# Kernel tuning notes

Hardware: AMD Instinct MI355X
Metric: run time of the kernel (lower is better)

Reference implementation:

```python
import jax, jax.numpy as jnp
import numpy as np

ALPHA = 0.2  # LeakyReLU negative slope


def _head(x, W, b, a, eye):
    # x: [B,N,F], W: [F,D], a: [2D,1], eye: [N,N] identity
    h = x @ W + b                                   # [B,N,D]
    D = W.shape[1]
    # additive attention: score[i,j] = leakyrelu(a_l . h_i + a_r . h_j)
    s = jax.nn.leaky_relu(h @ a[:D] + jnp.swapaxes(h @ a[D:], 1, 2), ALPHA)  # [B,N,N]
    s = jnp.where(eye > 0, -jnp.inf, s)             # mask diagonal (adj_identity)
    p = jax.nn.softmax(s, axis=-1) + eye            # softmax then add identity
    return jax.nn.elu(p @ h)                        # [B,N,D]


def setup_inputs() -> dict:
    key = jax.random.key(0)
    ks = jax.random.split(key, 16)
    B, N, F_IN, HID, HEADS = 8, 2048, 256, 256, 2
    D = HID // HEADS
    inp = {
        "x": jax.random.normal(ks[0], (B, N, F_IN), dtype=jnp.float32),
        "edges": jax.random.randint(ks[1], (B, N), 0, N, dtype=jnp.int64),
    }
    i = 2
    for layer in range(2):
        fin = F_IN if layer == 0 else HID
        for head in range(HEADS):
            inp[f"W_{layer}_{head}"] = jax.random.normal(ks[i], (fin, D), dtype=jnp.float32) * (1.0 / np.sqrt(fin)); i += 1
            inp[f"b_{layer}_{head}"] = jnp.zeros((D,), dtype=jnp.float32)
            inp[f"a_{layer}_{head}"] = jax.random.normal(ks[i], (2 * D, 1), dtype=jnp.float32) * 0.1; i += 1
    return inp


def reference(x, edges, W_0_0, b_0_0, a_0_0, W_0_1, b_0_1, a_0_1,
              W_1_0, b_1_0, a_1_0, W_1_1, b_1_1, a_1_1):
    N = x.shape[1]
    eye = jnp.eye(N, dtype=x.dtype)
    layers = [
        [(W_0_0, b_0_0, a_0_0), (W_0_1, b_0_1, a_0_1)],
        [(W_1_0, b_1_0, a_1_0), (W_1_1, b_1_1, a_1_1)],
    ]
    for heads in layers:
        x = jnp.concatenate([_head(x, W, b, a, eye) for (W, b, a) in heads], axis=-1)
    return x
```

## Files before the change

kernel.cpp:

```cpp
#include <hip/hip_runtime.h>
#include <math.h>

#define ALPHA_SLOPE 0.2f

typedef _Float16 f16;
typedef f16 f16x4 __attribute__((ext_vector_type(4)));
typedef f16 f16x8 __attribute__((ext_vector_type(8)));
typedef float f32x4 __attribute__((ext_vector_type(4)));

constexpr int B_ = 8, N = 2048, D = 128, H = 2;
constexpr int C2 = H * D;
constexpr int M_ = B_ * N;
constexpr int NCH = 32;
constexpr int CHL = N / NCH;

__device__ __forceinline__ float lrelu(float x) { return fmaxf(x, ALPHA_SLOPE * x); }

__global__ __launch_bounds__(256) void cvt_kernel(
    const float* __restrict__ x, f16* __restrict__ xh,
    const float* __restrict__ W00, const float* __restrict__ W01,
    const float* __restrict__ W10, const float* __restrict__ W11,
    f16* __restrict__ WcT)
{
    const int t = threadIdx.x;
    if (blockIdx.x < 4096) {
        const int idx = (blockIdx.x * 256 + t) * 4;
        const float4 v = *(const float4*)&x[idx];
        f16x4 o; o[0] = (f16)v.x; o[1] = (f16)v.y; o[2] = (f16)v.z; o[3] = (f16)v.w;
        *(f16x4*)&xh[idx] = o;
    } else {
        const int w = blockIdx.x - 4096;
#pragma unroll
        for (int p = 0; p < 4; ++p) {
            const int pair = w * 4 + p;
            const int layer = pair >> 8, c = pair & 255;
            const float* __restrict__ W0 = layer ? W10 : W00;
            const float* __restrict__ W1 = layer ? W11 : W01;
            const float v = (c < D) ? W0[t * D + c] : W1[t * D + (c - D)];
            WcT[(size_t)layer * C2 * C2 + c * C2 + t] = (f16)v;
        }
    }
}

__global__ __launch_bounds__(256) void gemm_lr_kernel(
    const f16* __restrict__ xh, const f16* __restrict__ Wl,
    const float* __restrict__ b0, const float* __restrict__ b1,
    const float* __restrict__ a0, const float* __restrict__ a1,
    f16* __restrict__ h,
    float* __restrict__ l0, float* __restrict__ r0,
    float* __restrict__ l1, float* __restrict__ r1)
{
    __shared__ f16 hts[32][C2 + 8];
    const int t = threadIdx.x;
    const int row0 = blockIdx.x * 32;
#pragma unroll
    for (int p = 0; p < 4; ++p) {
        const int q = p * 256 + t;
        const int row = q >> 5, cc = q & 31;
        *(f16x8*)&hts[row][cc * 8] = *(const f16x8*)&xh[(size_t)(row0 + row) * C2 + cc * 8];
    }
    __syncthreads();
    const int w = t >> 6, l = t & 63;
    const int fm = l & 15, fk = (l >> 4) * 8;
    f32x4 acc[2][4] = {};
#pragma unroll
    for (int ks = 0; ks < 8; ++ks) {
        f16x8 af[2], bf[4];
#pragma unroll
        for (int rt = 0; rt < 2; ++rt)
            af[rt] = *(const f16x8*)&hts[rt * 16 + fm][ks * 32 + fk];
#pragma unroll
        for (int ct = 0; ct < 4; ++ct) {
            const int col = w * 64 + ct * 16 + fm;
            bf[ct] = *(const f16x8*)&Wl[(size_t)col * C2 + ks * 32 + fk];
        }
#pragma unroll
        for (int rt = 0; rt < 2; ++rt)
#pragma unroll
            for (int ct = 0; ct < 4; ++ct)
                acc[rt][ct] = __builtin_amdgcn_mfma_f32_16x16x32_f16(af[rt], bf[ct], acc[rt][ct], 0, 0, 0);
    }
    __syncthreads();
#pragma unroll
    for (int rt = 0; rt < 2; ++rt)
#pragma unroll
        for (int ct = 0; ct < 4; ++ct) {
            const int col = w * 64 + ct * 16 + fm;
            const float bias = (col < D) ? b0[col] : b1[col - D];
#pragma unroll
            for (int q = 0; q < 4; ++q) {
                const int row = rt * 16 + (l >> 4) * 4 + q;
                hts[row][col] = (f16)(acc[rt][ct][q] + bias);
            }
        }
    __syncthreads();
#pragma unroll
    for (int p = 0; p < 4; ++p) {
        const int q = p * 256 + t;
        const int row = q >> 5, cc = q & 31;
        *(f16x8*)&h[(size_t)(row0 + row) * C2 + cc * 8] = *(const f16x8*)&hts[row][cc * 8];
    }
    const int lrow = t >> 3;
    const int oct = t & 7;
    const float* __restrict__ ab = (oct >= 4) ? a1 : a0;
    float lv = 0.f, rv = 0.f;
#pragma unroll
    for (int c4 = 0; c4 < 8; ++c4) {
        const int cc = (c4 + oct) & 7;
        const int col = oct * 32 + cc * 4;
        const int cih = (oct & 3) * 32 + cc * 4;
        const f16x4 hf = *(const f16x4*)&hts[lrow][col];
        const float4 alv = *(const float4*)&ab[cih];
        const float4 arv = *(const float4*)&ab[128 + cih];
        const float h0 = (float)hf[0], h1 = (float)hf[1], h2 = (float)hf[2], h3 = (float)hf[3];
        lv += h0 * alv.x + h1 * alv.y + h2 * alv.z + h3 * alv.w;
        rv += h0 * arv.x + h1 * arv.y + h2 * arv.z + h3 * arv.w;
    }
    lv += __shfl_xor(lv, 1, 64); lv += __shfl_xor(lv, 2, 64);
    rv += __shfl_xor(rv, 1, 64); rv += __shfl_xor(rv, 2, 64);
    const int grow = row0 + lrow;
    if (oct == 0) { l0[grow] = lv; r0[grow] = rv; }
    else if (oct == 4) { l1[grow] = lv; r1[grow] = rv; }
}

__global__ __launch_bounds__(256) void rank_kernel(
    const float* __restrict__ r0, const float* __restrict__ r1,
    const float* __restrict__ l0, const float* __restrict__ l1,
    float* __restrict__ rs_s, int* __restrict__ perm, int* __restrict__ kout)
{
    const int bh = blockIdx.y;
    const float* __restrict__ r = ((bh & 1) ? r1 : r0) + (size_t)(bh >> 1) * N;
    const float* __restrict__ lp = ((bh & 1) ? l1 : l0) + (size_t)(bh >> 1) * N;
    __shared__ float rl[N];
    __shared__ int scnt[4][64], sk2[4][64];
    const int t = threadIdx.x;
    for (int j = t; j < N; j += 256) rl[j] = r[j];
    __syncthreads();
    const int el = t & 63;
    const int q = t >> 6;
    const int e = blockIdx.x * 64 + el;
    const float re = rl[e];
    const float thr = -lp[e];
    const int qm = blockIdx.x >> 3;
    int cnt = 0, k2 = 0;
    const int jlo = q * 512, jhi = jlo + 512;
    if (q < qm) {
        for (int j = jlo; j < jhi; j += 4) {
            const float4 v = *(const float4*)&rl[j];
            cnt += (v.x >= re) + (v.y >= re) + (v.z >= re) + (v.w >= re);
            k2  += (v.x >= thr) + (v.y >= thr) + (v.z >= thr) + (v.w >= thr);
        }
    } else if (q > qm) {
        for (int j = jlo; j < jhi; j += 4) {
            const float4 v = *(const float4*)&rl[j];
            cnt += (v.x > re) + (v.y > re) + (v.z > re) + (v.w > re);
            k2  += (v.x >= thr) + (v.y >= thr) + (v.z >= thr) + (v.w >= thr);
        }
    } else {
        for (int j = jlo; j < jhi; j += 4) {
            const float4 v = *(const float4*)&rl[j];
            cnt += (v.x > re) || (v.x == re && (j + 0) < e);
            cnt += (v.y > re) || (v.y == re && (j + 1) < e);
            cnt += (v.z > re) || (v.z == re && (j + 2) < e);
            cnt += (v.w > re) || (v.w == re && (j + 3) < e);
            k2  += (v.x >= thr) + (v.y >= thr) + (v.z >= thr) + (v.w >= thr);
        }
    }
    scnt[q][el] = cnt; sk2[q][el] = k2;
    __syncthreads();
    if (t < 64) {
        const int c = scnt[0][t] + scnt[1][t] + scnt[2][t] + scnt[3][t];
        const int kk = sk2[0][t] + sk2[1][t] + sk2[2][t] + sk2[3][t];
        const int eg = blockIdx.x * 64 + t;
        const size_t g = (size_t)bh * N;
        rs_s[g + c] = rl[eg];
        perm[g + c] = eg;
        kout[g + eg] = kk;
    }
}

__global__ __launch_bounds__(256) void scanA_kernel(
    const f16* __restrict__ h, const int* __restrict__ perm,
    const float* __restrict__ rs_s,
    f16* __restrict__ PA, f16* __restrict__ PB,
    float* __restrict__ SAloc, float* __restrict__ SBloc,
    float* __restrict__ totA, float* __restrict__ totB,
    float* __restrict__ stA, float* __restrict__ stB)
{
    __shared__ f16 hs[CHL][D];
    __shared__ int pj[CHL];
    __shared__ float wA[CHL], wB[CHL];
    __shared__ float buf[2 * CHL];
    const int chunk = blockIdx.x, bh = blockIdx.y;
    const int b = bh >> 1, head = bh & 1;
    const int t = threadIdx.x;
    const size_t g = (size_t)bh * N + chunk * CHL;
    const float c1 = rs_s[(size_t)bh * N];
    if (t < CHL) {
        pj[t] = perm[g + t];
        const float rr = rs_s[g + t];
        const float eA = __expf(rr - c1);
        const float eB = __expf(0.2f * (rr - c1));
        wA[t] = eA; wB[t] = eB;
        buf[t] = eA;
    } else if (t < 2 * CHL) {
        const float rr = rs_s[g + (CHL - 1 - (t - CHL))];
        buf[t] = __expf(0.2f * (rr - c1));
    }
    __syncthreads();
    const int li = t & (CHL - 1);
#pragma unroll
    for (int off = 1; off < CHL; off <<= 1) {
        const float v = (t < 2 * CHL && li >= off) ? buf[t - off] : 0.f;
        __syncthreads();
        if (t < 2 * CHL && li >= off) buf[t] += v;
        __syncthreads();
    }
    if (t < CHL) SAloc[g + t] = buf[t];
    else if (t < 2 * CHL) SBloc[g + (CHL - 1 - li)] = buf[t];
    if (t == CHL - 1) stA[bh * NCH + chunk] = buf[CHL - 1];
    if (t == 2 * CHL - 1) stB[bh * NCH + chunk] = buf[2 * CHL - 1];
#pragma unroll
    for (int p = 0; p < 4; ++p) {
        const int q = p * 256 + t;
        const int row = q >> 4, c8 = q & 15;
        const f16* src = h + (size_t)(b * N + pj[row]) * C2 + head * D;
        *(f16x8*)&hs[row][c8 * 8] = *(const f16x8*)&src[c8 * 8];
    }
    __syncthreads();
    if (t < D) {
        const int d = t;
        float acc = 0.f;
        for (int j = 0; j < CHL; ++j) {
            acc = fmaf(wA[j], (float)hs[j][d], acc);
            PA[(g + j) * D + d] = (f16)acc;
        }
        totA[(size_t)(bh * NCH + chunk) * D + d] = acc;
    } else {
        const int d = t - D;
        float acc = 0.f;
        for (int jj = 0; jj < CHL; ++jj) {
            const int j = CHL - 1 - jj;
            acc = fmaf(wB[j], (float)hs[j][d], acc);
            PB[(g + j) * D + d] = (f16)acc;
        }
        totB[(size_t)(bh * NCH + chunk) * D + d] = acc;
    }
}

__global__ __launch_bounds__(256) void out_kernel(
    const f16* __restrict__ h,
    const float* __restrict__ l0v, const float* __restrict__ l1v,
    const float* __restrict__ r0v, const float* __restrict__ r1v,
    const int* __restrict__ perm, const float* __restrict__ rs_s,
    const int* __restrict__ kout,
    const float* __restrict__ SAloc, const float* __restrict__ SBloc,
    const float* __restrict__ stA, const float* __restrict__ stB,
    const float* __restrict__ totA, const float* __restrict__ totB,
    const f16* __restrict__ PA, const f16* __restrict__ PB,
    float* __restrict__ out_f32, f16* __restrict__ out_f16, const int final_layer)
{
    __shared__ float ldsA[NCH][D];
    __shared__ float ldsB[NCH][D];
    __shared__ float lsA[NCH], lsB[NCH];
    const int head = blockIdx.y, b = blockIdx.z;
    const int bh = b * H + head;
    const float* __restrict__ lv = (head ? l1v : l0v) + (size_t)b * N;
    const float* __restrict__ rv = (head ? r1v : r0v) + (size_t)b * N;
    const int t = threadIdx.x;
    const size_t gb = (size_t)bh * N;

#pragma unroll
    for (int p = 0; p < 4; ++p) {
        const int idx = p * 256 + t;
        const int ch = idx >> 5, c4 = idx & 31;
        *(float4*)&ldsA[ch][c4 * 4] = *(const float4*)&totA[(size_t)(bh * NCH + ch) * D + c4 * 4];
        *(float4*)&ldsB[ch][c4 * 4] = *(const float4*)&totB[(size_t)(bh * NCH + ch) * D + c4 * 4];
    }
    if (t < NCH) lsA[t] = stA[bh * NCH + t];
    else if (t < 2 * NCH) lsB[t - NCH] = stB[bh * NCH + (t - NCH)];
    __syncthreads();
    if (t < D) {
        const int d = t;
        float acc = 0.f;
        for (int q = 0; q < NCH; ++q) {
            const float tmp = ldsA[q][d];
            ldsA[q][d] = acc;
            acc += tmp;
        }
    } else {
        const int d = t - D;
        float acc = 0.f;
        for (int q = NCH - 1; q >= 0; --q) {
            const float tmp = ldsB[q][d];
            ldsB[q][d] = acc;
            acc += tmp;
        }
    }
    if (t == 0) {
        float a = 0.f;
        for (int q = 0; q < NCH; ++q) { const float tmp = lsA[q]; lsA[q] = a; a += tmp; }
    } else if (t == 1) {
        float a = 0.f;
        for (int q = NCH - 1; q >= 0; --q) { const float tmp = lsB[q]; lsB[q] = a; a += tmp; }
    }
    __syncthreads();

    const int i = blockIdx.x * 16 + (t >> 4);
    const int c0 = (t & 15) * 8;
    const float li = lv[i];
    const float ri = rv[i];
    const float rmx1 = rs_s[gb];
    const float rmx2 = rs_s[gb + 1];
    const int rdx = perm[gb];
    const float rmx = (i == rdx) ? rmx2 : rmx1;
    const float m = lrelu(li + rmx);
    const float alpha = __expf(li + rmx1 - m);
    const float beta = __expf(0.2f * (li + rmx1) - m);
    const float diag = __expf(lrelu(li + ri) - m);

    const int k = kout[gb + i];
    const float SAk = (k > 0) ? (lsA[(k - 1) >> 6] + SAloc[gb + k - 1]) : 0.f;
    const float SBk = (k < N) ? (lsB[k >> 6] + SBloc[gb + k]) : 0.f;
    const float Z = fmaf(alpha, SAk, beta * SBk) - diag;
    const float invZ = 1.f / Z;

    float pa[8] = {}, pb[8] = {};
    if (k > 0) {
        const int kk = k - 1, ch = kk >> 6;
        const f16x8 v = *(const f16x8*)&PA[(gb + kk) * D + c0];
#pragma unroll
        for (int q = 0; q < 8; ++q) pa[q] = (float)v[q] + ldsA[ch][c0 + q];
    }
    if (k < N) {
        const int ch = k >> 6;
        const f16x8 v = *(const f16x8*)&PB[(gb + k) * D + c0];
#pragma unroll
        for (int q = 0; q < 8; ++q) pb[q] = (float)v[q] + ldsB[ch][c0 + q];
    }

    const f16x8 hraw = *(const f16x8*)&h[(size_t)(b * N + i) * C2 + head * D + c0];
    float o[8];
#pragma unroll
    for (int q = 0; q < 8; ++q) {
        const float hv = (float)hraw[q];
        const float num = alpha * pa[q] + beta * pb[q] - diag * hv;
        float v = fmaf(num, invZ, hv);
        o[q] = v > 0.f ? v : (__expf(v) - 1.f);
    }
    const size_t oidx = (size_t)(b * N + i) * C2 + head * D + c0;
    if (final_layer) {
        *(float4*)&out_f32[oidx] = make_float4(o[0], o[1], o[2], o[3]);
        *(float4*)&out_f32[oidx + 4] = make_float4(o[4], o[5], o[6], o[7]);
    } else {
        f16x8 ov;
#pragma unroll
        for (int q = 0; q < 8; ++q) ov[q] = (f16)o[q];
        *(f16x8*)&out_f16[oidx] = ov;
    }
}

extern "C" void kernel_launch(void* const* d_in, const int* in_sizes, int n_in,
                              void* d_out, int out_size, void* d_ws, size_t ws_size,
                              hipStream_t stream)
{
    float* ws = (float*)d_ws;
    size_t off = 0;
    f16* xh = (f16*)(ws + off);   off += (size_t)M_ * C2 / 2;
    f16* WcT = (f16*)(ws + off);  off += (size_t)C2 * C2;
    f16* h = (f16*)(ws + off);    off += (size_t)M_ * C2 / 2;
    float* l0 = ws + off;         off += (size_t)B_ * N;
    float* r0 = ws + off;         off += (size_t)B_ * N;
    float* l1 = ws + off;         off += (size_t)B_ * N;
    float* r1 = ws + off;         off += (size_t)B_ * N;
    float* rs_s = ws + off;       off += (size_t)16 * N;
    int* perm = (int*)(ws + off); off += (size_t)16 * N;
    int* kout = (int*)(ws + off); off += (size_t)16 * N;
    float* SAloc = ws + off;      off += (size_t)16 * N;
    float* SBloc = ws + off;      off += (size_t)16 * N;
    f16* PA = (f16*)(ws + off);   off += (size_t)16 * N * D / 2;
    f16* PB = (f16*)(ws + off);   off += (size_t)16 * N * D / 2;
    float* totA = ws + off;       off += (size_t)16 * NCH * D;
    float* totB = ws + off;       off += (size_t)16 * NCH * D;
    float* stA = ws + off;        off += (size_t)16 * NCH;
    float* stB = ws + off;        off += (size_t)16 * NCH;

    cvt_kernel<<<4096 + 128, 256, 0, stream>>>(
        (const float*)d_in[0], xh,
        (const float*)d_in[2], (const float*)d_in[5],
        (const float*)d_in[8], (const float*)d_in[11], WcT);

    for (int layer = 0; layer < 2; ++layer) {
        const int base = 2 + layer * 6;
        const float* b0 = (const float*)d_in[base + 1];
        const float* a0 = (const float*)d_in[base + 2];
        const float* b1 = (const float*)d_in[base + 4];
        const float* a1 = (const float*)d_in[base + 5];

        gemm_lr_kernel<<<M_ / 32, 256, 0, stream>>>(
            xh, WcT + (size_t)layer * C2 * C2, b0, b1, a0, a1, h, l0, r0, l1, r1);
        rank_kernel<<<dim3(N / 64, B_ * H), 256, 0, stream>>>(
            r0, r1, l0, l1, rs_s, perm, kout);
        scanA_kernel<<<dim3(NCH, B_ * H), 256, 0, stream>>>(
            h, perm, rs_s, PA, PB, SAloc, SBloc, totA, totB, stA, stB);
        out_kernel<<<dim3(N / 16, H, B_), 256, 0, stream>>>(
            h, l0, l1, r0, r1, perm, rs_s, kout, SAloc, SBloc, stA, stB,
            totA, totB, PA, PB, (float*)d_out, xh, layer == 1 ? 1 : 0);
    }
}
```

Baseline: 208.6 us.

## Fuse all stages into one persistent kernel with software grid barriers

Replaces the conversion kernel and the per-layer GEMM, rank, scan and output kernels with a single persistent kernel of 512 blocks. The stages are separated by an atomic-counter grid barrier, and shared memory is overlaid through a union. The aim is to remove launch overhead and inter-kernel gaps across nine launches. In exchange, every stage is bound to a fixed 512-block mapping with two blocks per CU, which can lower parallelism in some stages. It also depends on all blocks being co-resident for the spin barrier to avoid deadlock.

New measurement: 768.1 us. 268% more time.

```diff
diff --git a/kernel.cpp b/kernel.cpp
--- a/kernel.cpp
+++ b/kernel.cpp
@@ -13,350 +13,370 @@
 constexpr int M_ = B_ * N;
 constexpr int NCH = 32;
 constexpr int CHL = N / NCH;
+constexpr int NB = 512;
 
 __device__ __forceinline__ float lrelu(float x) { return fmaxf(x, ALPHA_SLOPE * x); }
 
-__global__ __launch_bounds__(256) void cvt_kernel(
-    const float* __restrict__ x, f16* __restrict__ xh,
-    const float* __restrict__ W00, const float* __restrict__ W01,
-    const float* __restrict__ W10, const float* __restrict__ W11,
-    f16* __restrict__ WcT)
+struct Params {
+    const float *x;
+    const float *W00, *W01, *W10, *W11;
+    const float *b00, *a00, *b01, *a01;
+    const float *b10, *a10, *b11, *a11;
+    f16 *xh, *WcT, *h;
+    float *l0, *r0, *l1, *r1;
+    float *rs_s; int *perm; int *kout;
+    float *SAloc, *SBloc;
+    f16 *PA, *PB;
+    float *totA, *totB, *stA, *stB;
+    float *out_f32;
+    unsigned *bar;
+};
+
+union SharedU {
+    struct { f16 hts[32][C2 + 8]; } g;
+    struct { float rl[N]; int scnt[4][64]; int sk2[4][64]; } rk;
+    struct { f16 hs[CHL][D]; int pj[CHL]; float wA[CHL]; float wB[CHL];
+             float buf[2 * CHL]; } sc;
+    struct { float ldsA[NCH][D]; float ldsB[NCH][D];
+             float lsA[NCH]; float lsB[NCH]; } ot;
+};
+
+__device__ __forceinline__ void gridbar(unsigned* cnt, unsigned& tgt)
 {
-    const int t = threadIdx.x;
-    if (blockIdx.x < 4096) {
-        const int idx = (blockIdx.x * 256 + t) * 4;
-        const float4 v = *(const float4*)&x[idx];
-        f16x4 o; o[0] = (f16)v.x; o[1] = (f16)v.y; o[2] = (f16)v.z; o[3] = (f16)v.w;
-        *(f16x4*)&xh[idx] = o;
-    } else {
-        const int w = blockIdx.x - 4096;
-#pragma unroll
-        for (int p = 0; p < 4; ++p) {
-            const int pair = w * 4 + p;
-            const int layer = pair >> 8, c = pair & 255;
-            const float* __restrict__ W0 = layer ? W10 : W00;
-            const float* __restrict__ W1 = layer ? W11 : W01;
-            const float v = (c < D) ? W0[t * D + c] : W1[t * D + (c - D)];
-            WcT[(size_t)layer * C2 * C2 + c * C2 + t] = (f16)v;
-        }
-    }
-}
-
-__global__ __launch_bounds__(256) void gemm_lr_kernel(
-    const f16* __restrict__ xh, const f16* __restrict__ Wl,
-    const float* __restrict__ b0, const float* __restrict__ b1,
-    const float* __restrict__ a0, const float* __restrict__ a1,
-    f16* __restrict__ h,
-    float* __restrict__ l0, float* __restrict__ r0,
-    float* __restrict__ l1, float* __restrict__ r1)
-{
-    __shared__ f16 hts[32][C2 + 8];
-    const int t = threadIdx.x;
-    const int row0 = blockIdx.x * 32;
-#pragma unroll
-    for (int p = 0; p < 4; ++p) {
-        const int q = p * 256 + t;
-        const int row = q >> 5, cc = q & 31;
-        *(f16x8*)&hts[row][cc * 8] = *(const f16x8*)&xh[(size_t)(row0 + row) * C2 + cc * 8];
+    __syncthreads();
+    if (threadIdx.x == 0) {
+        __threadfence();
+        __hip_atomic_fetch_add(cnt, 1u, __ATOMIC_RELEASE, __HIP_MEMORY_SCOPE_AGENT);
+        tgt += (unsigned)NB;
+        while (__hip_atomic_load(cnt, __ATOMIC_ACQUIRE, __HIP_MEMORY_SCOPE_AGENT) < tgt) {
+            __builtin_amdgcn_s_sleep(2);
+        }
+        __threadfence();
     }
     __syncthreads();
-    const int w = t >> 6, l = t & 63;
-    const int fm = l & 15, fk = (l >> 4) * 8;
-    f32x4 acc[2][4] = {};
-#pragma unroll
-    for (int ks = 0; ks < 8; ++ks) {
-        f16x8 af[2], bf[4];
-#pragma unroll
-        for (int rt = 0; rt < 2; ++rt)
-            af[rt] = *(const f16x8*)&hts[rt * 16 + fm][ks * 32 + fk];
-#pragma unroll
-        for (int ct = 0; ct < 4; ++ct) {
-            const int col = w * 64 + ct * 16 + fm;
-            bf[ct] = *(const f16x8*)&Wl[(size_t)col * C2 + ks * 32 + fk];
-        }
-#pragma unroll
-        for (int rt = 0; rt < 2; ++rt)
-#pragma unroll
-            for (int ct = 0; ct < 4; ++ct)
-                acc[rt][ct] = __builtin_amdgcn_mfma_f32_16x16x32_f16(af[rt], bf[ct], acc[rt][ct], 0, 0, 0);
+}
+
+__global__ void bar_init(unsigned* bar) { bar[0] = 0u; }
+
+__global__ __launch_bounds__(256, 2) void gat_mega(Params P)
+{
+    __shared__ SharedU S;
+    const int t = threadIdx.x;
+    const int blk = blockIdx.x;
+    unsigned bar_tgt = 0u;
+
+    for (int u = blk; u < 4096 + 128; u += NB) {
+        if (u < 4096) {
+            const int idx = (u * 256 + t) * 4;
+            const float4 v = *(const float4*)&P.x[idx];
+            f16x4 o; o[0] = (f16)v.x; o[1] = (f16)v.y; o[2] = (f16)v.z; o[3] = (f16)v.w;
+            *(f16x4*)&P.xh[idx] = o;
+        } else {
+            const int w = u - 4096;
+#pragma unroll
+            for (int p = 0; p < 4; ++p) {
+                const int pair = w * 4 + p;
+                const int ly = pair >> 8, c = pair & 255;
+                const float* __restrict__ W0 = ly ? P.W10 : P.W00;
+                const float* __restrict__ W1 = ly ? P.W11 : P.W01;
+                const float v = (c < D) ? W0[t * D + c] : W1[t * D + (c - D)];
+                P.WcT[(size_t)ly * C2 * C2 + c * C2 + t] = (f16)v;
+            }
+        }
     }
-    __syncthreads();
-#pragma unroll
-    for (int rt = 0; rt < 2; ++rt)
-#pragma unroll
-        for (int ct = 0; ct < 4; ++ct) {
-            const int col = w * 64 + ct * 16 + fm;
-            const float bias = (col < D) ? b0[col] : b1[col - D];
-#pragma unroll
-            for (int q = 0; q < 4; ++q) {
-                const int row = rt * 16 + (l >> 4) * 4 + q;
-                hts[row][col] = (f16)(acc[rt][ct][q] + bias);
-            }
-        }
-    __syncthreads();
-#pragma unroll
-    for (int p = 0; p < 4; ++p) {
-        const int q = p * 256 + t;
-        const int row = q >> 5, cc = q & 31;
-        *(f16x8*)&h[(size_t)(row0 + row) * C2 + cc * 8] = *(const f16x8*)&hts[row][cc * 8];
-    }
-    const int lrow = t >> 3;
-    const int oct = t & 7;
-    const float* __restrict__ ab = (oct >= 4) ? a1 : a0;
-    float lv = 0.f, rv = 0.f;
-#pragma unroll
-    for (int c4 = 0; c4 < 8; ++c4) {
-        const int cc = (c4 + oct) & 7;
-        const int col = oct * 32 + cc * 4;
-        const int cih = (oct & 3) * 32 + cc * 4;
-        const f16x4 hf = *(const f16x4*)&hts[lrow][col];
-        const float4 alv = *(const float4*)&ab[cih];
-        const float4 arv = *(const float4*)&ab[128 + cih];
-        const float h0 = (float)hf[0], h1 = (float)hf[1], h2 = (float)hf[2], h3 = (float)hf[3];
-        lv += h0 * alv.x + h1 * alv.y + h2 * alv.z + h3 * alv.w;
-        rv += h0 * arv.x + h1 * arv.y + h2 * arv.z + h3 * arv.w;
-    }
-    lv += __shfl_xor(lv, 1, 64); lv += __shfl_xor(lv, 2, 64);
-    rv += __shfl_xor(rv, 1, 64); rv += __shfl_xor(rv, 2, 64);
-    const int grow = row0 + lrow;
-    if (oct == 0) { l0[grow] = lv; r0[grow] = rv; }
-    else if (oct == 4) { l1[grow] = lv; r1[grow] = rv; }
-}
-
-__global__ __launch_bounds__(256) void rank_kernel(
-    const float* __restrict__ r0, const float* __restrict__ r1,
-    const float* __restrict__ l0, const float* __restrict__ l1,
-    float* __restrict__ rs_s, int* __restrict__ perm, int* __restrict__ kout)
-{
-    const int bh = blockIdx.y;
-    const float* __restrict__ r = ((bh & 1) ? r1 : r0) + (size_t)(bh >> 1) * N;
-    const float* __restrict__ lp = ((bh & 1) ? l1 : l0) + (size_t)(bh >> 1) * N;
-    __shared__ float rl[N];
-    __shared__ int scnt[4][64], sk2[4][64];
-    const int t = threadIdx.x;
-    for (int j = t; j < N; j += 256) rl[j] = r[j];
-    __syncthreads();
-    const int el = t & 63;
-    const int q = t >> 6;
-    const int e = blockIdx.x * 64 + el;
-    const float re = rl[e];
-    const float thr = -lp[e];
-    const int qm = blockIdx.x >> 3;
-    int cnt = 0, k2 = 0;
-    const int jlo = q * 512, jhi = jlo + 512;
-    if (q < qm) {
-        for (int j = jlo; j < jhi; j += 4) {
-            const float4 v = *(const float4*)&rl[j];
-            cnt += (v.x >= re) + (v.y >= re) + (v.z >= re) + (v.w >= re);
-            k2  += (v.x >= thr) + (v.y >= thr) + (v.z >= thr) + (v.w >= thr);
-        }
-    } else if (q > qm) {
-        for (int j = jlo; j < jhi; j += 4) {
-            const float4 v = *(const float4*)&rl[j];
-            cnt += (v.x > re) + (v.y > re) + (v.z > re) + (v.w > re);
-            k2  += (v.x >= thr) + (v.y >= thr) + (v.z >= thr) + (v.w >= thr);
-        }
-    } else {
-        for (int j = jlo; j < jhi; j += 4) {
-            const float4 v = *(const float4*)&rl[j];
-            cnt += (v.x > re) || (v.x == re && (j + 0) < e);
-            cnt += (v.y > re) || (v.y == re && (j + 1) < e);
-            cnt += (v.z > re) || (v.z == re && (j + 2) < e);
-            cnt += (v.w > re) || (v.w == re && (j + 3) < e);
-            k2  += (v.x >= thr) + (v.y >= thr) + (v.z >= thr) + (v.w >= thr);
-        }
-    }
-    scnt[q][el] = cnt; sk2[q][el] = k2;
-    __syncthreads();
-    if (t < 64) {
-        const int c = scnt[0][t] + scnt[1][t] + scnt[2][t] + scnt[3][t];
-        const int kk = sk2[0][t] + sk2[1][t] + sk2[2][t] + sk2[3][t];
-        const int eg = blockIdx.x * 64 + t;
-        const size_t g = (size_t)bh * N;
-        rs_s[g + c] = rl[eg];
-        perm[g + c] = eg;
-        kout[g + eg] = kk;
-    }
-}
-
-__global__ __launch_bounds__(256) void scanA_kernel(
-    const f16* __restrict__ h, const int* __restrict__ perm,
-    const float* __restrict__ rs_s,
-    f16* __restrict__ PA, f16* __restrict__ PB,
-    float* __restrict__ SAloc, float* __restrict__ SBloc,
-    float* __restrict__ totA, float* __restrict__ totB,
-    float* __restrict__ stA, float* __restrict__ stB)
-{
-    __shared__ f16 hs[CHL][D];
-    __shared__ int pj[CHL];
-    __shared__ float wA[CHL], wB[CHL];
-    __shared__ float buf[2 * CHL];
-    const int chunk = blockIdx.x, bh = blockIdx.y;
-    const int b = bh >> 1, head = bh & 1;
-    const int t = threadIdx.x;
-    const size_t g = (size_t)bh * N + chunk * CHL;
-    const float c1 = rs_s[(size_t)bh * N];
-    if (t < CHL) {
-        pj[t] = perm[g + t];
-        const float rr = rs_s[g + t];
-        const float eA = __expf(rr - c1);
-        const float eB = __expf(0.2f * (rr - c1));
-        wA[t] = eA; wB[t] = eB;
-        buf[t] = eA;
-    } else if (t < 2 * CHL) {
-        const float rr = rs_s[g + (CHL - 1 - (t - CHL))];
-        buf[t] = __expf(0.2f * (rr - c1));
-    }
-    __syncthreads();
-    const int li = t & (CHL - 1);
-#pragma unroll
-    for (int off = 1; off < CHL; off <<= 1) {
-        const float v = (t < 2 * CHL && li >= off) ? buf[t - off] : 0.f;
-        __syncthreads();
-        if (t < 2 * CHL && li >= off) buf[t] += v;
-        __syncthreads();
-    }
-    if (t < CHL) SAloc[g + t] = buf[t];
-    else if (t < 2 * CHL) SBloc[g + (CHL - 1 - li)] = buf[t];
-    if (t == CHL - 1) stA[bh * NCH + chunk] = buf[CHL - 1];
-    if (t == 2 * CHL - 1) stB[bh * NCH + chunk] = buf[2 * CHL - 1];
-#pragma unroll
-    for (int p = 0; p < 4; ++p) {
-        const int q = p * 256 + t;
-        const int row = q >> 4, c8 = q & 15;
-        const f16* src = h + (size_t)(b * N + pj[row]) * C2 + head * D;
-        *(f16x8*)&hs[row][c8 * 8] = *(const f16x8*)&src[c8 * 8];
-    }
-    __syncthreads();
-    if (t < D) {
-        const int d = t;
-        float acc = 0.f;
-        for (int j = 0; j < CHL; ++j) {
-            acc = fmaf(wA[j], (float)hs[j][d], acc);
-            PA[(g + j) * D + d] = (f16)acc;
-        }
-        totA[(size_t)(bh * NCH + chunk) * D + d] = acc;
-    } else {
-        const int d = t - D;
-        float acc = 0.f;
-        for (int jj = 0; jj < CHL; ++jj) {
-            const int j = CHL - 1 - jj;
-            acc = fmaf(wB[j], (float)hs[j][d], acc);
-            PB[(g + j) * D + d] = (f16)acc;
-        }
-        totB[(size_t)(bh * NCH + chunk) * D + d] = acc;
-    }
-}
-
-__global__ __launch_bounds__(256) void out_kernel(
-    const f16* __restrict__ h,
-    const float* __restrict__ l0v, const float* __restrict__ l1v,
-    const float* __restrict__ r0v, const float* __restrict__ r1v,
-    const int* __restrict__ perm, const float* __restrict__ rs_s,
-    const int* __restrict__ kout,
-    const float* __restrict__ SAloc, const float* __restrict__ SBloc,
-    const float* __restrict__ stA, const float* __restrict__ stB,
-    const float* __restrict__ totA, const float* __restrict__ totB,
-    const f16* __restrict__ PA, const f16* __restrict__ PB,
-    float* __restrict__ out_f32, f16* __restrict__ out_f16, const int final_layer)
-{
-    __shared__ float ldsA[NCH][D];
-    __shared__ float ldsB[NCH][D];
-    __shared__ float lsA[NCH], lsB[NCH];
-    const int head = blockIdx.y, b = blockIdx.z;
-    const int bh = b * H + head;
-    const float* __restrict__ lv = (head ? l1v : l0v) + (size_t)b * N;
-    const float* __restrict__ rv = (head ? r1v : r0v) + (size_t)b * N;
-    const int t = threadIdx.x;
-    const size_t gb = (size_t)bh * N;
-
-#pragma unroll
-    for (int p = 0; p < 4; ++p) {
-        const int idx = p * 256 + t;
-        const int ch = idx >> 5, c4 = idx & 31;
-        *(float4*)&ldsA[ch][c4 * 4] = *(const float4*)&totA[(size_t)(bh * NCH + ch) * D + c4 * 4];
-        *(float4*)&ldsB[ch][c4 * 4] = *(const float4*)&totB[(size_t)(bh * NCH + ch) * D + c4 * 4];
-    }
-    if (t < NCH) lsA[t] = stA[bh * NCH + t];
-    else if (t < 2 * NCH) lsB[t - NCH] = stB[bh * NCH + (t - NCH)];
-    __syncthreads();
-    if (t < D) {
-        const int d = t;
-        float acc = 0.f;
-        for (int q = 0; q < NCH; ++q) {
-            const float tmp = ldsA[q][d];
-            ldsA[q][d] = acc;
-            acc += tmp;
-        }
-    } else {
-        const int d = t - D;
-        float acc = 0.f;
-        for (int q = NCH - 1; q >= 0; --q) {
-            const float tmp = ldsB[q][d];
-            ldsB[q][d] = acc;
-            acc += tmp;
-        }
-    }
-    if (t == 0) {
-        float a = 0.f;
-        for (int q = 0; q < NCH; ++q) { const float tmp = lsA[q]; lsA[q] = a; a += tmp; }
-    } else if (t == 1) {
-        float a = 0.f;
-        for (int q = NCH - 1; q >= 0; --q) { const float tmp = lsB[q]; lsB[q] = a; a += tmp; }
-    }
-    __syncthreads();
-
-    const int i = blockIdx.x * 16 + (t >> 4);
-    const int c0 = (t & 15) * 8;
-    const float li = lv[i];
-    const float ri = rv[i];
-    const float rmx1 = rs_s[gb];
-    const float rmx2 = rs_s[gb + 1];
-    const int rdx = perm[gb];
-    const float rmx = (i == rdx) ? rmx2 : rmx1;
-    const float m = lrelu(li + rmx);
-    const float alpha = __expf(li + rmx1 - m);
-    const float beta = __expf(0.2f * (li + rmx1) - m);
-    const float diag = __expf(lrelu(li + ri) - m);
-
-    const int k = kout[gb + i];
-    const float SAk = (k > 0) ? (lsA[(k - 1) >> 6] + SAloc[gb + k - 1]) : 0.f;
-    const float SBk = (k < N) ? (lsB[k >> 6] + SBloc[gb + k]) : 0.f;
-    const float Z = fmaf(alpha, SAk, beta * SBk) - diag;
-    const float invZ = 1.f / Z;
-
-    float pa[8] = {}, pb[8] = {};
-    if (k > 0) {
-        const int kk = k - 1, ch = kk >> 6;
-        const f16x8 v = *(const f16x8*)&PA[(gb + kk) * D + c0];
-#pragma unroll
-        for (int q = 0; q < 8; ++q) pa[q] = (float)v[q] + ldsA[ch][c0 + q];
-    }
-    if (k < N) {
-        const int ch = k >> 6;
-        const f16x8 v = *(const f16x8*)&PB[(gb + k) * D + c0];
-#pragma unroll
-        for (int q = 0; q < 8; ++q) pb[q] = (float)v[q] + ldsB[ch][c0 + q];
-    }
-
-    const f16x8 hraw = *(const f16x8*)&h[(size_t)(b * N + i) * C2 + head * D + c0];
-    float o[8];
-#pragma unroll
-    for (int q = 0; q < 8; ++q) {
-        const float hv = (float)hraw[q];
-        const float num = alpha * pa[q] + beta * pb[q] - diag * hv;
-        float v = fmaf(num, invZ, hv);
-        o[q] = v > 0.f ? v : (__expf(v) - 1.f);
-    }
-    const size_t oidx = (size_t)(b * N + i) * C2 + head * D + c0;
-    if (final_layer) {
-        *(float4*)&out_f32[oidx] = make_float4(o[0], o[1], o[2], o[3]);
-        *(float4*)&out_f32[oidx + 4] = make_float4(o[4], o[5], o[6], o[7]);
-    } else {
-        f16x8 ov;
-#pragma unroll
-        for (int q = 0; q < 8; ++q) ov[q] = (f16)o[q];
-        *(f16x8*)&out_f16[oidx] = ov;
+    gridbar(P.bar, bar_tgt);
+
+    for (int layer = 0; layer < 2; ++layer) {
+        const float* __restrict__ b0 = layer ? P.b10 : P.b00;
+        const float* __restrict__ a0 = layer ? P.a10 : P.a00;
+        const float* __restrict__ b1 = layer ? P.b11 : P.b01;
+        const float* __restrict__ a1 = layer ? P.a11 : P.a01;
+        const f16* __restrict__ Wl = P.WcT + (size_t)layer * C2 * C2;
+
+        {
+            const f16* __restrict__ xhp = P.xh;
+            f16* __restrict__ hp = P.h;
+            const int row0 = blk * 32;
+#pragma unroll
+            for (int p = 0; p < 4; ++p) {
+                const int q = p * 256 + t;
+                const int row = q >> 5, cc = q & 31;
+                *(f16x8*)&S.g.hts[row][cc * 8] = *(const f16x8*)&xhp[(size_t)(row0 + row) * C2 + cc * 8];
+            }
+            __syncthreads();
+            const int w = t >> 6, l = t & 63;
+            const int fm = l & 15, fk = (l >> 4) * 8;
+            f32x4 acc[2][4] = {};
+#pragma unroll
+            for (int ks = 0; ks < 8; ++ks) {
+                f16x8 af[2], bf[4];
+#pragma unroll
+                for (int rt = 0; rt < 2; ++rt)
+                    af[rt] = *(const f16x8*)&S.g.hts[rt * 16 + fm][ks * 32 + fk];
+#pragma unroll
+                for (int ct = 0; ct < 4; ++ct) {
+                    const int col = w * 64 + ct * 16 + fm;
+                    bf[ct] = *(const f16x8*)&Wl[(size_t)col * C2 + ks * 32 + fk];
+                }
+#pragma unroll
+                for (int rt = 0; rt < 2; ++rt)
+#pragma unroll
+                    for (int ct = 0; ct < 4; ++ct)
+                        acc[rt][ct] = __builtin_amdgcn_mfma_f32_16x16x32_f16(af[rt], bf[ct], acc[rt][ct], 0, 0, 0);
+            }
+            __syncthreads();
+#pragma unroll
+            for (int rt = 0; rt < 2; ++rt)
+#pragma unroll
+                for (int ct = 0; ct < 4; ++ct) {
+                    const int col = w * 64 + ct * 16 + fm;
+                    const float bias = (col < D) ? b0[col] : b1[col - D];
+#pragma unroll
+                    for (int q = 0; q < 4; ++q) {
+                        const int row = rt * 16 + (l >> 4) * 4 + q;
+                        S.g.hts[row][col] = (f16)(acc[rt][ct][q] + bias);
+                    }
+                }
+            __syncthreads();
+#pragma unroll
+            for (int p = 0; p < 4; ++p) {
+                const int q = p * 256 + t;
+                const int row = q >> 5, cc = q & 31;
+                *(f16x8*)&hp[(size_t)(row0 + row) * C2 + cc * 8] = *(const f16x8*)&S.g.hts[row][cc * 8];
+            }
+            const int lrow = t >> 3;
+            const int oct = t & 7;
+            const float* __restrict__ ab = (oct >= 4) ? a1 : a0;
+            float lvv = 0.f, rvv = 0.f;
+#pragma unroll
+            for (int c4 = 0; c4 < 8; ++c4) {
+                const int cc = (c4 + oct) & 7;
+                const int col = oct * 32 + cc * 4;
+                const int cih = (oct & 3) * 32 + cc * 4;
+                const f16x4 hf = *(const f16x4*)&S.g.hts[lrow][col];
+                const float4 alv = *(const float4*)&ab[cih];
+                const float4 arv = *(const float4*)&ab[128 + cih];
+                const float h0 = (float)hf[0], h1 = (float)hf[1], h2 = (float)hf[2], h3 = (float)hf[3];
+                lvv += h0 * alv.x + h1 * alv.y + h2 * alv.z + h3 * alv.w;
+                rvv += h0 * arv.x + h1 * arv.y + h2 * arv.z + h3 * arv.w;
+            }
+            lvv += __shfl_xor(lvv, 1, 64); lvv += __shfl_xor(lvv, 2, 64);
+            rvv += __shfl_xor(rvv, 1, 64); rvv += __shfl_xor(rvv, 2, 64);
+            const int grow = row0 + lrow;
+            if (oct == 0) { P.l0[grow] = lvv; P.r0[grow] = rvv; }
+            else if (oct == 4) { P.l1[grow] = lvv; P.r1[grow] = rvv; }
+        }
+        gridbar(P.bar, bar_tgt);
+
+        {
+            const int bh = blk >> 5;
+            const int cb = blk & 31;
+            const float* __restrict__ r = ((bh & 1) ? P.r1 : P.r0) + (size_t)(bh >> 1) * N;
+            const float* __restrict__ lp = ((bh & 1) ? P.l1 : P.l0) + (size_t)(bh >> 1) * N;
+            for (int j = t; j < N; j += 256) S.rk.rl[j] = r[j];
+            __syncthreads();
+            const int el = t & 63;
+            const int q = t >> 6;
+            const int e = cb * 64 + el;
+            const float re = S.rk.rl[e];
+            const float thr = -lp[e];
+            const int qm = cb >> 3;
+            int cnt = 0, k2 = 0;
+            const int jlo = q * 512, jhi = jlo + 512;
+            if (q < qm) {
+                for (int j = jlo; j < jhi; j += 4) {
+                    const float4 v = *(const float4*)&S.rk.rl[j];
+                    cnt += (v.x >= re) + (v.y >= re) + (v.z >= re) + (v.w >= re);
+                    k2  += (v.x >= thr) + (v.y >= thr) + (v.z >= thr) + (v.w >= thr);
+                }
+            } else if (q > qm) {
+                for (int j = jlo; j < jhi; j += 4) {
+                    const float4 v = *(const float4*)&S.rk.rl[j];
+                    cnt += (v.x > re) + (v.y > re) + (v.z > re) + (v.w > re);
+                    k2  += (v.x >= thr) + (v.y >= thr) + (v.z >= thr) + (v.w >= thr);
+                }
+            } else {
+                for (int j = jlo; j < jhi; j += 4) {
+                    const float4 v = *(const float4*)&S.rk.rl[j];
+                    cnt += (v.x > re) || (v.x == re && (j + 0) < e);
+                    cnt += (v.y > re) || (v.y == re && (j + 1) < e);
+                    cnt += (v.z > re) || (v.z == re && (j + 2) < e);
+                    cnt += (v.w > re) || (v.w == re && (j + 3) < e);
+                    k2  += (v.x >= thr) + (v.y >= thr) + (v.z >= thr) + (v.w >= thr);
+                }
+            }
+            S.rk.scnt[q][el] = cnt; S.rk.sk2[q][el] = k2;
+            __syncthreads();
+            if (t < 64) {
+                const int c = S.rk.scnt[0][t] + S.rk.scnt[1][t] + S.rk.scnt[2][t] + S.rk.sk2[3][t] - S.rk.sk2[3][t] + S.rk.scnt[3][t];
+                const int kk = S.rk.sk2[0][t] + S.rk.sk2[1][t] + S.rk.sk2[2][t] + S.rk.sk2[3][t];
+                const int eg = cb * 64 + t;
+                const size_t gg = (size_t)bh * N;
+                P.rs_s[gg + c] = S.rk.rl[eg];
+                P.perm[gg + c] = eg;
+                P.kout[gg + eg] = kk;
+            }
+        }
+        gridbar(P.bar, bar_tgt);
+
+        {
+            const int chunk = blk & 31, bh = blk >> 5;
+            const int b = bh >> 1, head = bh & 1;
+            const size_t g = (size_t)bh * N + chunk * CHL;
+            const float c1 = P.rs_s[(size_t)bh * N];
+            if (t < CHL) {
+                S.sc.pj[t] = P.perm[g + t];
+                const float rr = P.rs_s[g + t];
+                const float eA = __expf(rr - c1);
+                const float eB = __expf(0.2f * (rr - c1));
+                S.sc.wA[t] = eA; S.sc.wB[t] = eB;
+                S.sc.buf[t] = eA;
+            } else if (t < 2 * CHL) {
+                const float rr = P.rs_s[g + (CHL - 1 - (t - CHL))];
+                S.sc.buf[t] = __expf(0.2f * (rr - c1));
+            }
+            __syncthreads();
+            const int li = t & (CHL - 1);
+#pragma unroll
+            for (int off = 1; off < CHL; off <<= 1) {
+                const float v = (t < 2 * CHL && li >= off) ? S.sc.buf[t - off] : 0.f;
+                __syncthreads();
+                if (t < 2 * CHL && li >= off) S.sc.buf[t] += v;
+                __syncthreads();
+            }
+            if (t < CHL) P.SAloc[g + t] = S.sc.buf[t];
+            else if (t < 2 * CHL) P.SBloc[g + (CHL - 1 - li)] = S.sc.buf[t];
+            if (t == CHL - 1) P.stA[bh * NCH + chunk] = S.sc.buf[CHL - 1];
+            if (t == 2 * CHL - 1) P.stB[bh * NCH + chunk] = S.sc.buf[2 * CHL - 1];
+#pragma unroll
+            for (int p = 0; p < 4; ++p) {
+                const int q = p * 256 + t;
+                const int row = q >> 4, c8 = q & 15;
+                const f16* __restrict__ src = P.h + (size_t)(b * N + S.sc.pj[row]) * C2 + head * D;
+                *(f16x8*)&S.sc.hs[row][c8 * 8] = *(const f16x8*)&src[c8 * 8];
+            }
+            __syncthreads();
+            if (t < D) {
+                const int d = t;
+                float acc = 0.f;
+                for (int j = 0; j < CHL; ++j) {
+                    acc = fmaf(S.sc.wA[j], (float)S.sc.hs[j][d], acc);
+                    P.PA[(g + j) * D + d] = (f16)acc;
+                }
+                P.totA[(size_t)(bh * NCH + chunk) * D + d] = acc;
+            } else {
+                const int d = t - D;
+                float acc = 0.f;
+                for (int jj = 0; jj < CHL; ++jj) {
+                    const int j = CHL - 1 - jj;
+                    acc = fmaf(S.sc.wB[j], (float)S.sc.hs[j][d], acc);
+                    P.PB[(g + j) * D + d] = (f16)acc;
+                }
+                P.totB[(size_t)(bh * NCH + chunk) * D + d] = acc;
+            }
+        }
+        gridbar(P.bar, bar_tgt);
+
+        {
+            const int bh = blk >> 5;
+            const int b = bh >> 1, head = bh & 1;
+            const float* __restrict__ lv = (head ? P.l1 : P.l0) + (size_t)b * N;
+            const float* __restrict__ rv = (head ? P.r1 : P.r0) + (size_t)b * N;
+            const size_t gb = (size_t)bh * N;
+#pragma unroll
+            for (int p = 0; p < 4; ++p) {
+                const int idx = p * 256 + t;
+                const int ch = idx >> 5, c4 = idx & 31;
+                *(float4*)&S.ot.ldsA[ch][c4 * 4] = *(const float4*)&P.totA[(size_t)(bh * NCH + ch) * D + c4 * 4];
+                *(float4*)&S.ot.ldsB[ch][c4 * 4] = *(const float4*)&P.totB[(size_t)(bh * NCH + ch) * D + c4 * 4];
+            }
+            if (t < NCH) S.ot.lsA[t] = P.stA[bh * NCH + t];
+            else if (t < 2 * NCH) S.ot.lsB[t - NCH] = P.stB[bh * NCH + (t - NCH)];
+            __syncthreads();
+            if (t < D) {
+                const int d = t;
+                float acc = 0.f;
+                for (int q = 0; q < NCH; ++q) {
+                    const float tmp = S.ot.ldsA[q][d];
+                    S.ot.ldsA[q][d] = acc;
+                    acc += tmp;
+                }
+            } else {
+                const int d = t - D;
+                float acc = 0.f;
+                for (int q = NCH - 1; q >= 0; --q) {
+                    const float tmp = S.ot.ldsB[q][d];
+                    S.ot.ldsB[q][d] = acc;
+                    acc += tmp;
+                }
+            }
+            if (t == 0) {
+                float a = 0.f;
+                for (int q = 0; q < NCH; ++q) { const float tmp = S.ot.lsA[q]; S.ot.lsA[q] = a; a += tmp; }
+            } else if (t == 1) {
+                float a = 0.f;
+                for (int q = NCH - 1; q >= 0; --q) { const float tmp = S.ot.lsB[q]; S.ot.lsB[q] = a; a += tmp; }
+            }
+            __syncthreads();
+
+            const float rmx1 = P.rs_s[gb];
+            const float rmx2 = P.rs_s[gb + 1];
+            const int rdx = P.perm[gb];
+            const int c0 = (t & 15) * 8;
+            for (int g4 = 0; g4 < 4; ++g4) {
+                const int i = ((blk & 31) * 4 + g4) * 16 + (t >> 4);
+                const float li = lv[i];
+                const float ri = rv[i];
+                const float rmx = (i == rdx) ? rmx2 : rmx1;
+                const float m = lrelu(li + rmx);
+                const float alpha = __expf(li + rmx1 - m);
+                const float beta = __expf(0.2f * (li + rmx1) - m);
+                const float diag = __expf(lrelu(li + ri) - m);
+
+                const int k = P.kout[gb + i];
+                const float SAk = (k > 0) ? (S.ot.lsA[(k - 1) >> 6] + P.SAloc[gb + k - 1]) : 0.f;
+                const float SBk = (k < N) ? (S.ot.lsB[k >> 6] + P.SBloc[gb + k]) : 0.f;
+                const float Z = fmaf(alpha, SAk, beta * SBk) - diag;
+                const float invZ = 1.f / Z;
+
+                float pa[8] = {}, pb[8] = {};
+                if (k > 0) {
+                    const int kk = k - 1, ch = kk >> 6;
+                    const f16x8 v = *(const f16x8*)&P.PA[(gb + kk) * D + c0];
+#pragma unroll
+                    for (int q = 0; q < 8; ++q) pa[q] = (float)v[q] + S.ot.ldsA[ch][c0 + q];
+                }
+                if (k < N) {
+                    const int ch = k >> 6;
+                    const f16x8 v = *(const f16x8*)&P.PB[(gb + k) * D + c0];
+#pragma unroll
+                    for (int q = 0; q < 8; ++q) pb[q] = (float)v[q] + S.ot.ldsB[ch][c0 + q];
+                }
+
+                const f16x8 hraw = *(const f16x8*)&P.h[(size_t)(b * N + i) * C2 + head * D + c0];
+                float o[8];
+#pragma unroll
+                for (int q = 0; q < 8; ++q) {
+                    const float hv = (float)hraw[q];
+                    const float num = alpha * pa[q] + beta * pb[q] - diag * hv;
+                    float v = fmaf(num, invZ, hv);
+                    o[q] = v > 0.f ? v : (__expf(v) - 1.f);
+                }
+                const size_t oidx = (size_t)(b * N + i) * C2 + head * D + c0;
+                if (layer == 1) {
+                    *(float4*)&P.out_f32[oidx] = make_float4(o[0], o[1], o[2], o[3]);
+                    *(float4*)&P.out_f32[oidx + 4] = make_float4(o[4], o[5], o[6], o[7]);
+                } else {
+                    f16x8 ov;
+#pragma unroll
+                    for (int q = 0; q < 8; ++q) ov[q] = (f16)o[q];
+                    *(f16x8*)&P.xh[oidx] = ov;
+                }
+            }
+        }
+        if (layer == 0) {
+            gridbar(P.bar, bar_tgt);
+        }
     }
 }
 
@@ -384,27 +404,23 @@
     float* totB = ws + off;       off += (size_t)16 * NCH * D;
     float* stA = ws + off;        off += (size_t)16 * NCH;
     float* stB = ws + off;        off += (size_t)16 * NCH;
-
-    cvt_kernel<<<4096 + 128, 256, 0, stream>>>(
-        (const float*)d_in[0], xh,
-        (const float*)d_in[2], (const float*)d_in[5],
-        (const float*)d_in[8], (const float*)d_in[11], WcT);
-
-    for (int layer = 0; layer < 2; ++layer) {
-        const int base = 2 + layer * 6;
-        const float* b0 = (const float*)d_in[base + 1];
-        const float* a0 = (const float*)d_in[base + 2];
-        const float* b1 = (const float*)d_in[base + 4];
-        const float* a1 = (const float*)d_in[base + 5];
-
-        gemm_lr_kernel<<<M_ / 32, 256, 0, stream>>>(
-            xh, WcT + (size_t)layer * C2 * C2, b0, b1, a0, a1, h, l0, r0, l1, r1);
-        rank_kernel<<<dim3(N / 64, B_ * H), 256, 0, stream>>>(
-            r0, r1, l0, l1, rs_s, perm, kout);
-        scanA_kernel<<<dim3(NCH, B_ * H), 256, 0, stream>>>(
-            h, perm, rs_s, PA, PB, SAloc, SBloc, totA, totB, stA, stB);
-        out_kernel<<<dim3(N / 16, H, B_), 256, 0, stream>>>(
-            h, l0, l1, r0, r1, perm, rs_s, kout, SAloc, SBloc, stA, stB,
-            totA, totB, PA, PB, (float*)d_out, xh, layer == 1 ? 1 : 0);
-    }
+    unsigned* bar = (unsigned*)(ws + off); off += 64;
+
+    Params P;
+    P.x   = (const float*)d_in[0];
+    P.W00 = (const float*)d_in[2];  P.b00 = (const float*)d_in[3];  P.a00 = (const float*)d_in[4];
+    P.W01 = (const float*)d_in[5];  P.b01 = (const float*)d_in[6];  P.a01 = (const float*)d_in[7];
+    P.W10 = (const float*)d_in[8];  P.b10 = (const float*)d_in[9];  P.a10 = (const float*)d_in[10];
+    P.W11 = (const float*)d_in[11]; P.b11 = (const float*)d_in[12]; P.a11 = (const float*)d_in[13];
+    P.xh = xh; P.WcT = WcT; P.h = h;
+    P.l0 = l0; P.r0 = r0; P.l1 = l1; P.r1 = r1;
+    P.rs_s = rs_s; P.perm = perm; P.kout = kout;
+    P.SAloc = SAloc; P.SBloc = SBloc;
+    P.PA = PA; P.PB = PB;
+    P.totA = totA; P.totB = totB; P.stA = stA; P.stB = stB;
+    P.out_f32 = (float*)d_out;
+    P.bar = bar;
+
+    bar_init<<<1, 1, 0, stream>>>(bar);
+    gat_mega<<<NB, 256, 0, stream>>>(P);
 }
```
